# Performance work log

Hardware: AMD Instinct MI355X
Metric: run time of the kernel (lower is better)

The kernel has to match this reference:

```python
import jax, jax.numpy as jnp
import numpy as np

B, S, E, H = 1, 4096, 768, 12
D = E // H  # head_dim = 64


def setup_inputs() -> dict:
    key = jax.random.key(0)
    ks = jax.random.split(key, 9)
    s = 1.0 / np.sqrt(E)
    return {
        "x": jax.random.normal(ks[0], (B, S, E), dtype=jnp.float32),
        "Wq": jax.random.uniform(ks[1], (E, E), jnp.float32, -s, s),
        "bq": jax.random.uniform(ks[2], (E,), jnp.float32, -s, s),
        "Wk": jax.random.uniform(ks[3], (E, E), jnp.float32, -s, s),
        "bk": jax.random.uniform(ks[4], (E,), jnp.float32, -s, s),
        "Wv": jax.random.uniform(ks[5], (E, E), jnp.float32, -s, s),
        "bv": jax.random.uniform(ks[6], (E,), jnp.float32, -s, s),
        "Wo": jax.random.uniform(ks[7], (E, E), jnp.float32, -s, s),
        "bo": jax.random.uniform(ks[8], (E,), jnp.float32, -s, s),
    }


def reference(x, Wq, bq, Wk, bk, Wv, bv, Wo, bo):
    b, s, e = x.shape
    # QKV projections, split heads -> [b, h, s, d]
    def split(t):
        return t.reshape(b, s, H, D).transpose(0, 2, 1, 3)
    q = split(x @ Wq.T + bq)
    k = split(x @ Wk.T + bk)
    v = split(x @ Wv.T + bv)
    scores = jnp.einsum("bhqd,bhkd->bhqk", q, k) / jnp.sqrt(jnp.float32(D))
    attn = jax.nn.softmax(scores, axis=-1)  # dropout is identity in eval
    out = jnp.einsum("bhqk,bhkd->bhqd", attn, v)
    out = out.transpose(0, 2, 1, 3).reshape(b, s, e)
    return out @ Wo.T + bo
```

## Files before the change

kernel.cpp:

```cpp
#include <hip/hip_runtime.h>
#include <hip/hip_bf16.h>
#include <math.h>

#define SEQ 4096
#define EDIM 768
#define NHEAD 12
#define HDIM 64
#define SE (SEQ * EDIM)
#define WMAT (EDIM * EDIM)
#define QSCALE 0.180336880111f

typedef __attribute__((ext_vector_type(8))) __bf16 bf16x8;
typedef __attribute__((ext_vector_type(4))) float f32x4;
typedef __attribute__((ext_vector_type(8))) unsigned short u16x8;
typedef unsigned short ushort_t;
typedef unsigned int uint_t;

#define MFMA16(a, b, c) __builtin_amdgcn_mfma_f32_16x16x32_bf16(a, b, c, 0, 0, 0)
#define GLOAD_LDS16(g, l)                                          \
  __builtin_amdgcn_global_load_lds(                                \
      (const __attribute__((address_space(1))) void*)(g),          \
      (__attribute__((address_space(3))) void*)(l), 16, 0, 0)

__device__ __forceinline__ unsigned short bfbits(float x) {
  return __builtin_bit_cast(unsigned short, (__bf16)x);
}
__device__ __forceinline__ void split1(float x, unsigned short* h,
                                       unsigned short* l) {
  __bf16 hb = (__bf16)x;
  *h = __builtin_bit_cast(unsigned short, hb);
  *l = __builtin_bit_cast(unsigned short, (__bf16)(x - (float)hb));
}
__device__ __forceinline__ bf16x8 ones8() {
  u16x8 u;
#pragma unroll
  for (int e = 0; e < 8; ++e) u[e] = 0x3F80;
  return __builtin_bit_cast(bf16x8, u);
}
__device__ __forceinline__ float exp2_hw(float x) {
  float r;
  asm("v_exp_f32 %0, %1" : "=v"(r) : "v"(x));
  return r;
}

__global__ __launch_bounds__(256) void wprep_kernel(
    const float* __restrict__ W0, const float* __restrict__ W1,
    const float* __restrict__ W2, const float* __restrict__ W3,
    ushort_t* __restrict__ WB, ushort_t* __restrict__ WOH,
    ushort_t* __restrict__ WOL) {
  const int m = blockIdx.y;
  const float* src = (m == 0) ? W0 : (m == 1) ? W1 : (m == 2) ? W2 : W3;
  const size_t i = ((size_t)blockIdx.x * 256 + threadIdx.x) * 8;
  float4 a = *(const float4*)(src + i);
  float4 b = *(const float4*)(src + i + 4);
  float fv[8] = {a.x, a.y, a.z, a.w, b.x, b.y, b.z, b.w};
  if (m < 3) {
    u16x8 hh;
#pragma unroll
    for (int e = 0; e < 8; ++e) hh[e] = bfbits(fv[e]);
    *(u16x8*)(WB + (size_t)m * WMAT + i) = hh;
  } else {
    u16x8 hh, ll;
#pragma unroll
    for (int e = 0; e < 8; ++e) {
      unsigned short x, y;
      split1(fv[e], &x, &y);
      hh[e] = x;
      ll[e] = y;
    }
    *(u16x8*)(WOH + i) = hh;
    *(u16x8*)(WOL + i) = ll;
  }
}

__global__ __launch_bounds__(256) void xprep_kernel(
    const float* __restrict__ x, ushort_t* __restrict__ xb) {
  const size_t i = ((size_t)blockIdx.x * 256 + threadIdx.x) * 8;
  float4 a = *(const float4*)(x + i);
  float4 b = *(const float4*)(x + i + 4);
  float fv[8] = {a.x, a.y, a.z, a.w, b.x, b.y, b.z, b.w};
  u16x8 hh;
#pragma unroll
  for (int e = 0; e < 8; ++e) hh[e] = bfbits(fv[e]);
  *(u16x8*)(xb + i) = hh;
}

__global__ __launch_bounds__(256) void vtrans_kernel(
    const ushort_t* __restrict__ VB, ushort_t* __restrict__ VT) {
  __shared__ ushort_t T[64][65];
  const int t = threadIdx.x;
  const int s0 = blockIdx.x * 64;
  const int hoff = blockIdx.y * 64;
  const int r = t >> 2, c = (t & 3) * 16;
  u16x8 a = *(const u16x8*)(VB + (size_t)(s0 + r) * EDIM + hoff + c);
  u16x8 b = *(const u16x8*)(VB + (size_t)(s0 + r) * EDIM + hoff + c + 8);
#pragma unroll
  for (int e = 0; e < 8; ++e) {
    T[r][c + e] = a[e];
    T[r][c + 8 + e] = b[e];
  }
  __syncthreads();
  u16x8 w0, w1;
#pragma unroll
  for (int e = 0; e < 8; ++e) {
    w0[e] = T[c + e][r];
    w1[e] = T[c + 8 + e][r];
  }
  *(u16x8*)(VT + (size_t)(hoff + r) * SEQ + s0 + c) = w0;
  *(u16x8*)(VT + (size_t)(hoff + r) * SEQ + s0 + c + 8) = w1;
}

__global__ __launch_bounds__(256) void qkv_kernel(
    const ushort_t* __restrict__ XB, const ushort_t* __restrict__ WB,
    const float* __restrict__ bq, const float* __restrict__ bk,
    const float* __restrict__ bv, ushort_t* __restrict__ QB,
    ushort_t* __restrict__ KB, ushort_t* __restrict__ VB) {
  __shared__ __align__(16) ushort_t AS[128][32];
  __shared__ __align__(16) ushort_t BS[128][32];

  const int z = blockIdx.z;
  const ushort_t* Bmat = WB + (size_t)z * WMAT;
  const float* bias = (z == 0) ? bq : (z == 1) ? bk : bv;
  ushort_t* outp = (z == 0) ? QB : (z == 1) ? KB : VB;
  const float scale = (z == 0) ? QSCALE : 1.0f;

  const int t = threadIdx.x;
  const int lane = t & 63;
  const int w = t >> 6;
  const int tn = t & 15;
  const int g = (t >> 4) & 3;
  const int wr = w >> 1, wc = w & 1;
  const int m0 = blockIdx.x * 128;
  const int n0 = blockIdx.y * 128;

  f32x4 acc[4][4];
#pragma unroll
  for (int mi = 0; mi < 4; ++mi)
#pragma unroll
    for (int nj = 0; nj < 4; ++nj) acc[mi][nj] = (f32x4){0.f, 0.f, 0.f, 0.f};

  const int crow = lane >> 2;
  const int ccol = (lane & 3) * 8;

  for (int k0 = 0; k0 < EDIM; k0 += 32) {
    __syncthreads();
#pragma unroll
    for (int i = 0; i < 2; ++i) {
      const int ch = w + 4 * i;
      const int row = ch * 16 + crow;
      GLOAD_LDS16(XB + (size_t)(m0 + row) * EDIM + k0 + ccol, &AS[ch * 16][0]);
      GLOAD_LDS16(Bmat + (size_t)(n0 + row) * EDIM + k0 + ccol, &BS[ch * 16][0]);
    }
    __syncthreads();

    bf16x8 ah[4], bh[4];
#pragma unroll
    for (int mi = 0; mi < 4; ++mi)
      ah[mi] = __builtin_bit_cast(
          bf16x8, *(const u16x8*)&AS[wr * 64 + mi * 16 + tn][8 * g]);
#pragma unroll
    for (int nj = 0; nj < 4; ++nj)
      bh[nj] = __builtin_bit_cast(
          bf16x8, *(const u16x8*)&BS[wc * 64 + nj * 16 + tn][8 * g]);
#pragma unroll
    for (int mi = 0; mi < 4; ++mi)
#pragma unroll
      for (int nj = 0; nj < 4; ++nj)
        acc[mi][nj] = MFMA16(ah[mi], bh[nj], acc[mi][nj]);
  }

#pragma unroll
  for (int mi = 0; mi < 4; ++mi) {
    const int rb = m0 + wr * 64 + mi * 16 + 4 * g;
#pragma unroll
    for (int nj = 0; nj < 4; ++nj) {
      const int col = n0 + wc * 64 + nj * 16 + tn;
      const float bb = bias[col];
#pragma unroll
      for (int r = 0; r < 4; ++r)
        outp[(size_t)(rb + r) * EDIM + col] =
            bfbits((acc[mi][nj][r] + bb) * scale);
    }
  }
}

__global__ __launch_bounds__(256) void proj_kernel(
    const ushort_t* __restrict__ Ah, const ushort_t* __restrict__ Al,
    const ushort_t* __restrict__ Bh, const ushort_t* __restrict__ Bl,
    const float* __restrict__ bias, float* __restrict__ outf) {
  __shared__ __align__(16) ushort_t AhS[128][32];
  __shared__ __align__(16) ushort_t AlS[128][32];
  __shared__ __align__(16) ushort_t BhS[128][32];
  __shared__ __align__(16) ushort_t BlS[128][32];

  const int t = threadIdx.x;
  const int lane = t & 63;
  const int w = t >> 6;
  const int tn = t & 15;
  const int g = (t >> 4) & 3;
  const int wr = w >> 1, wc = w & 1;
  const int m0 = blockIdx.x * 128;
  const int n0 = blockIdx.y * 128;

  f32x4 acc[4][4];
#pragma unroll
  for (int mi = 0; mi < 4; ++mi)
#pragma unroll
    for (int nj = 0; nj < 4; ++nj) acc[mi][nj] = (f32x4){0.f, 0.f, 0.f, 0.f};

  const int crow = lane >> 2;
  const int ccol = (lane & 3) * 8;

  for (int k0 = 0; k0 < EDIM; k0 += 32) {
    __syncthreads();
#pragma unroll
    for (int i = 0; i < 2; ++i) {
      const int ch = w + 4 * i;
      const int row = ch * 16 + crow;
      const size_t ga = (size_t)(m0 + row) * EDIM + k0 + ccol;
      const size_t gb = (size_t)(n0 + row) * EDIM + k0 + ccol;
      GLOAD_LDS16(Ah + ga, &AhS[ch * 16][0]);
      GLOAD_LDS16(Al + ga, &AlS[ch * 16][0]);
      GLOAD_LDS16(Bh + gb, &BhS[ch * 16][0]);
      GLOAD_LDS16(Bl + gb, &BlS[ch * 16][0]);
    }
    __syncthreads();

    bf16x8 ah[4], al[4], bh[4], bl[4];
#pragma unroll
    for (int mi = 0; mi < 4; ++mi) {
      ah[mi] = __builtin_bit_cast(
          bf16x8, *(const u16x8*)&AhS[wr * 64 + mi * 16 + tn][8 * g]);
      al[mi] = __builtin_bit_cast(
          bf16x8, *(const u16x8*)&AlS[wr * 64 + mi * 16 + tn][8 * g]);
    }
#pragma unroll
    for (int nj = 0; nj < 4; ++nj) {
      bh[nj] = __builtin_bit_cast(
          bf16x8, *(const u16x8*)&BhS[wc * 64 + nj * 16 + tn][8 * g]);
      bl[nj] = __builtin_bit_cast(
          bf16x8, *(const u16x8*)&BlS[wc * 64 + nj * 16 + tn][8 * g]);
    }
#pragma unroll
    for (int mi = 0; mi < 4; ++mi)
#pragma unroll
      for (int nj = 0; nj < 4; ++nj)
        acc[mi][nj] = MFMA16(ah[mi], bh[nj], acc[mi][nj]);
#pragma unroll
    for (int mi = 0; mi < 4; ++mi)
#pragma unroll
      for (int nj = 0; nj < 4; ++nj)
        acc[mi][nj] = MFMA16(al[mi], bh[nj], acc[mi][nj]);
#pragma unroll
    for (int mi = 0; mi < 4; ++mi)
#pragma unroll
      for (int nj = 0; nj < 4; ++nj)
        acc[mi][nj] = MFMA16(ah[mi], bl[nj], acc[mi][nj]);
  }

#pragma unroll
  for (int mi = 0; mi < 4; ++mi) {
    const int rb = m0 + wr * 64 + mi * 16 + 4 * g;
#pragma unroll
    for (int nj = 0; nj < 4; ++nj) {
      const int col = n0 + wc * 64 + nj * 16 + tn;
      const float bb = bias[col];
#pragma unroll
      for (int r = 0; r < 4; ++r)
        outf[(size_t)(rb + r) * EDIM + col] = acc[mi][nj][r] + bb;
    }
  }
}

__global__ __launch_bounds__(256) void attn_kernel(
    const ushort_t* __restrict__ QB, const ushort_t* __restrict__ KBg,
    const ushort_t* __restrict__ VTg, ushort_t* __restrict__ Ch_g,
    ushort_t* __restrict__ Cl_g) {
  __shared__ __align__(16) ushort_t KS[2][64][64];
  __shared__ __align__(16) ushort_t VS[2][64][64];
  __shared__ __align__(16) ushort_t Ps[4][16][72];

  const int t = threadIdx.x;
  const int lane = t & 63;
  const int tn = t & 15;
  const int g = (t >> 4) & 3;
  const int kg = g * 8;
  const int wid = t >> 6;
  const int h = blockIdx.y;
  const int q0 = blockIdx.x * 64;
  const int hoff = h * HDIM;

  bf16x8 qb[2];
  {
    const size_t qoff = (size_t)(q0 + 16 * wid + tn) * EDIM + hoff;
    qb[0] = __builtin_bit_cast(bf16x8, *(const u16x8*)(QB + qoff + kg));
    qb[1] = __builtin_bit_cast(bf16x8, *(const u16x8*)(QB + qoff + 32 + kg));
  }

  const int srow = lane >> 3;
  const int sxor = ((lane & 7) ^ srow) << 4;
  const int rswz = (tn & 7) << 4;
  const int off0 = (16 * g) ^ rswz;
  const int off1 = (64 + 16 * g) ^ rswz;

  const bf16x8 ones = ones8();
  f32x4 o[4], lsum;
#pragma unroll
  for (int j = 0; j < 4; ++j) o[j] = (f32x4){0.f, 0.f, 0.f, 0.f};
  lsum = (f32x4){0.f, 0.f, 0.f, 0.f};

#pragma unroll
  for (int c = 0; c < 2; ++c) {
    const int row = 16 * wid + 8 * c + srow;
    GLOAD_LDS16((const char*)(KBg + (size_t)row * EDIM + hoff) + sxor,
                &KS[0][16 * wid + 8 * c][0]);
    GLOAD_LDS16((const char*)(VTg + (size_t)(hoff + row) * SEQ) + sxor,
                &VS[0][16 * wid + 8 * c][0]);
  }

  for (int it = 0; it < SEQ / 64; ++it) {
    const int buf = it & 1;
    __syncthreads();

    if (it + 1 < SEQ / 64) {
      const int k0n = (it + 1) * 64;
#pragma unroll
      for (int c = 0; c < 2; ++c) {
        const int row = 16 * wid + 8 * c + srow;
        GLOAD_LDS16(
            (const char*)(KBg + (size_t)(k0n + row) * EDIM + hoff) + sxor,
            &KS[buf ^ 1][16 * wid + 8 * c][0]);
        GLOAD_LDS16(
            (const char*)(VTg + (size_t)(hoff + row) * SEQ + k0n) + sxor,
            &VS[buf ^ 1][16 * wid + 8 * c][0]);
      }
    }

    f32x4 s[4];
#pragma unroll
    for (int kb = 0; kb < 4; ++kb) {
      const char* krow = (const char*)&KS[buf][16 * kb + tn][0];
      const bf16x8 ka =
          __builtin_bit_cast(bf16x8, *(const u16x8*)(krow + off0));
      const bf16x8 kc =
          __builtin_bit_cast(bf16x8, *(const u16x8*)(krow + off1));
      s[kb] = (f32x4){0.f, 0.f, 0.f, 0.f};
      s[kb] = MFMA16(ka, qb[0], s[kb]);
      s[kb] = MFMA16(kc, qb[1], s[kb]);
    }

#pragma unroll
    for (int kb = 0; kb < 4; ++kb) {
      uint2 pk;
      pk.x = (uint_t)bfbits(exp2_hw(s[kb][0])) |
             ((uint_t)bfbits(exp2_hw(s[kb][1])) << 16);
      pk.y = (uint_t)bfbits(exp2_hw(s[kb][2])) |
             ((uint_t)bfbits(exp2_hw(s[kb][3])) << 16);
      *(uint2*)&Ps[wid][tn][16 * kb + 4 * g] = pk;
    }

    const bf16x8 pa0 =
        __builtin_bit_cast(bf16x8, *(const u16x8*)&Ps[wid][tn][kg]);
    const bf16x8 pa1 =
        __builtin_bit_cast(bf16x8, *(const u16x8*)&Ps[wid][tn][32 + kg]);

#pragma unroll
    for (int j = 0; j < 4; ++j) {
      const char* vrow = (const char*)&VS[buf][16 * j + tn][0];
      const bf16x8 v0 =
          __builtin_bit_cast(bf16x8, *(const u16x8*)(vrow + off0));
      const bf16x8 v1 =
          __builtin_bit_cast(bf16x8, *(const u16x8*)(vrow + off1));
      o[j] = MFMA16(pa0, v0, o[j]);
      o[j] = MFMA16(pa1, v1, o[j]);
    }
    lsum = MFMA16(pa0, ones, lsum);
    lsum = MFMA16(pa1, ones, lsum);
  }

#pragma unroll
  for (int r = 0; r < 4; ++r) {
    const float inv = 1.f / lsum[r];
#pragma unroll
    for (int j = 0; j < 4; ++j) {
      const float val = o[j][r] * inv;
      unsigned short hh, ll;
      split1(val, &hh, &ll);
      const size_t idx =
          (size_t)(q0 + 16 * wid + 4 * g + r) * EDIM + hoff + 16 * j + tn;
      Ch_g[idx] = hh;
      Cl_g[idx] = ll;
    }
  }
}

extern "C" void kernel_launch(void* const* d_in, const int* in_sizes, int n_in,
                              void* d_out, int out_size, void* d_ws,
                              size_t ws_size, hipStream_t stream) {
  const float* x  = (const float*)d_in[0];
  const float* Wq = (const float*)d_in[1];
  const float* bq = (const float*)d_in[2];
  const float* Wk = (const float*)d_in[3];
  const float* bk = (const float*)d_in[4];
  const float* Wv = (const float*)d_in[5];
  const float* bv = (const float*)d_in[6];
  const float* Wo = (const float*)d_in[7];
  const float* bo = (const float*)d_in[8];
  float* out = (float*)d_out;

  ushort_t* WB  = (ushort_t*)d_ws;
  ushort_t* WOH = WB + (size_t)3 * WMAT;
  ushort_t* WOL = WOH + (size_t)WMAT;
  ushort_t* XB  = WOL + (size_t)WMAT;
  ushort_t* QB  = XB + (size_t)SE;
  ushort_t* KB  = QB + (size_t)SE;
  ushort_t* VB  = KB + (size_t)SE;
  ushort_t* VT  = VB + (size_t)SE;
  ushort_t* CH  = VT + (size_t)SE;
  ushort_t* CL  = CH + (size_t)SE;

  dim3 gw(WMAT / 2048, 4);
  wprep_kernel<<<gw, 256, 0, stream>>>(Wq, Wk, Wv, Wo, WB, WOH, WOL);
  xprep_kernel<<<SE / 2048, 256, 0, stream>>>(x, XB);

  dim3 gq(SEQ / 128, EDIM / 128, 3);
  qkv_kernel<<<gq, 256, 0, stream>>>(XB, WB, bq, bk, bv, QB, KB, VB);

  dim3 gt(SEQ / 64, NHEAD);
  vtrans_kernel<<<gt, 256, 0, stream>>>(VB, VT);

  dim3 ga(SEQ / 64, NHEAD);
  attn_kernel<<<ga, 256, 0, stream>>>(QB, KB, VT, CH, CL);

  dim3 go(SEQ / 128, EDIM / 128);
  proj_kernel<<<go, 256, 0, stream>>>(CH, CL, WOH, WOL, bo, out);
}
```

Measured before the change: 167.4 us.

## Use 32x32 MFMA in attention with split-K waves; fuse V transpose into QKV epilogue

The attention kernel moves from 16x16x32 to 32x32x16 MFMA tiles. Each wave now handles 32 queries against half of each key block, and the two partial results are reduced through LDS at the end. The P fragment is built in registers with cvt_pk_bf16 and permlane32_swap, removing the per-iteration LDS round trip for P. The separate V transpose kernel is dropped: the QKV kernel writes V directly in transposed layout, which saves one launch and one pass over V in memory at the cost of strided 8-byte stores.

```diff
diff --git a/kernel.cpp b/kernel.cpp
--- a/kernel.cpp
+++ b/kernel.cpp
@@ -12,11 +12,14 @@
 
 typedef __attribute__((ext_vector_type(8))) __bf16 bf16x8;
 typedef __attribute__((ext_vector_type(4))) float f32x4;
+typedef __attribute__((ext_vector_type(16))) float f32x16;
 typedef __attribute__((ext_vector_type(8))) unsigned short u16x8;
+typedef __attribute__((ext_vector_type(4))) unsigned short u16x4;
 typedef unsigned short ushort_t;
 typedef unsigned int uint_t;
 
 #define MFMA16(a, b, c) __builtin_amdgcn_mfma_f32_16x16x32_bf16(a, b, c, 0, 0, 0)
+#define MFMA32(a, b, c) __builtin_amdgcn_mfma_f32_32x32x16_bf16(a, b, c, 0, 0, 0)
 #define GLOAD_LDS16(g, l)                                          \
   __builtin_amdgcn_global_load_lds(                                \
       (const __attribute__((address_space(1))) void*)(g),          \
@@ -40,6 +43,11 @@
 __device__ __forceinline__ float exp2_hw(float x) {
   float r;
   asm("v_exp_f32 %0, %1" : "=v"(r) : "v"(x));
+  return r;
+}
+__device__ __forceinline__ uint_t cvtpk(float a, float b) {
+  uint_t r;
+  asm("v_cvt_pk_bf16_f32 %0, %1, %2" : "=v"(r) : "v"(a), "v"(b));
   return r;
 }
 
@@ -85,43 +93,18 @@
   *(u16x8*)(xb + i) = hh;
 }
 
-__global__ __launch_bounds__(256) void vtrans_kernel(
-    const ushort_t* __restrict__ VB, ushort_t* __restrict__ VT) {
-  __shared__ ushort_t T[64][65];
-  const int t = threadIdx.x;
-  const int s0 = blockIdx.x * 64;
-  const int hoff = blockIdx.y * 64;
-  const int r = t >> 2, c = (t & 3) * 16;
-  u16x8 a = *(const u16x8*)(VB + (size_t)(s0 + r) * EDIM + hoff + c);
-  u16x8 b = *(const u16x8*)(VB + (size_t)(s0 + r) * EDIM + hoff + c + 8);
-#pragma unroll
-  for (int e = 0; e < 8; ++e) {
-    T[r][c + e] = a[e];
-    T[r][c + 8 + e] = b[e];
-  }
-  __syncthreads();
-  u16x8 w0, w1;
-#pragma unroll
-  for (int e = 0; e < 8; ++e) {
-    w0[e] = T[c + e][r];
-    w1[e] = T[c + 8 + e][r];
-  }
-  *(u16x8*)(VT + (size_t)(hoff + r) * SEQ + s0 + c) = w0;
-  *(u16x8*)(VT + (size_t)(hoff + r) * SEQ + s0 + c + 8) = w1;
-}
-
 __global__ __launch_bounds__(256) void qkv_kernel(
     const ushort_t* __restrict__ XB, const ushort_t* __restrict__ WB,
     const float* __restrict__ bq, const float* __restrict__ bk,
     const float* __restrict__ bv, ushort_t* __restrict__ QB,
-    ushort_t* __restrict__ KB, ushort_t* __restrict__ VB) {
+    ushort_t* __restrict__ KB, ushort_t* __restrict__ VT) {
   __shared__ __align__(16) ushort_t AS[128][32];
   __shared__ __align__(16) ushort_t BS[128][32];
 
   const int z = blockIdx.z;
   const ushort_t* Bmat = WB + (size_t)z * WMAT;
   const float* bias = (z == 0) ? bq : (z == 1) ? bk : bv;
-  ushort_t* outp = (z == 0) ? QB : (z == 1) ? KB : VB;
+  ushort_t* outp = (z == 0) ? QB : (z == 1) ? KB : VT;
   const float scale = (z == 0) ? QSCALE : 1.0f;
 
   const int t = threadIdx.x;
@@ -176,10 +159,17 @@
     for (int nj = 0; nj < 4; ++nj) {
       const int col = n0 + wc * 64 + nj * 16 + tn;
       const float bb = bias[col];
-#pragma unroll
-      for (int r = 0; r < 4; ++r)
-        outp[(size_t)(rb + r) * EDIM + col] =
-            bfbits((acc[mi][nj][r] + bb) * scale);
+      if (z == 2) {
+        u16x4 pk;
+#pragma unroll
+        for (int r = 0; r < 4; ++r) pk[r] = bfbits(acc[mi][nj][r] + bb);
+        *(u16x4*)(outp + (size_t)col * SEQ + rb) = pk;
+      } else {
+#pragma unroll
+        for (int r = 0; r < 4; ++r)
+          outp[(size_t)(rb + r) * EDIM + col] =
+              bfbits((acc[mi][nj][r] + bb) * scale);
+      }
     }
   }
 }
@@ -278,36 +268,37 @@
     ushort_t* __restrict__ Cl_g) {
   __shared__ __align__(16) ushort_t KS[2][64][64];
   __shared__ __align__(16) ushort_t VS[2][64][64];
-  __shared__ __align__(16) ushort_t Ps[4][16][72];
 
   const int t = threadIdx.x;
   const int lane = t & 63;
-  const int tn = t & 15;
-  const int g = (t >> 4) & 3;
-  const int kg = g * 8;
+  const int l31 = lane & 31;
+  const int hi = lane >> 5;
   const int wid = t >> 6;
-  const int h = blockIdx.y;
+  const int wq = wid & 1;
+  const int wk = wid >> 1;
   const int q0 = blockIdx.x * 64;
-  const int hoff = h * HDIM;
-
-  bf16x8 qb[2];
+  const int hoff = blockIdx.y * HDIM;
+
+  bf16x8 qf[4];
   {
-    const size_t qoff = (size_t)(q0 + 16 * wid + tn) * EDIM + hoff;
-    qb[0] = __builtin_bit_cast(bf16x8, *(const u16x8*)(QB + qoff + kg));
-    qb[1] = __builtin_bit_cast(bf16x8, *(const u16x8*)(QB + qoff + 32 + kg));
+    const ushort_t* qp =
+        QB + (size_t)(q0 + 32 * wq + l31) * EDIM + hoff + 8 * hi;
+#pragma unroll
+    for (int s4 = 0; s4 < 4; ++s4)
+      qf[s4] = __builtin_bit_cast(bf16x8, *(const u16x8*)(qp + 16 * s4));
   }
 
   const int srow = lane >> 3;
   const int sxor = ((lane & 7) ^ srow) << 4;
-  const int rswz = (tn & 7) << 4;
-  const int off0 = (16 * g) ^ rswz;
-  const int off1 = (64 + 16 * g) ^ rswz;
 
   const bf16x8 ones = ones8();
-  f32x4 o[4], lsum;
-#pragma unroll
-  for (int j = 0; j < 4; ++j) o[j] = (f32x4){0.f, 0.f, 0.f, 0.f};
-  lsum = (f32x4){0.f, 0.f, 0.f, 0.f};
+  f32x16 O0, O1, LS;
+#pragma unroll
+  for (int r = 0; r < 16; ++r) {
+    O0[r] = 0.f;
+    O1[r] = 0.f;
+    LS[r] = 0.f;
+  }
 
 #pragma unroll
   for (int c = 0; c < 2; ++c) {
@@ -317,6 +308,9 @@
     GLOAD_LDS16((const char*)(VTg + (size_t)(hoff + row) * SEQ) + sxor,
                 &VS[0][16 * wid + 8 * c][0]);
   }
+
+  const int krow = 32 * wk + l31;
+  const int kswz = (krow & 7) << 4;
 
   for (int it = 0; it < SEQ / 64; ++it) {
     const int buf = it & 1;
@@ -336,60 +330,105 @@
       }
     }
 
-    f32x4 s[4];
-#pragma unroll
-    for (int kb = 0; kb < 4; ++kb) {
-      const char* krow = (const char*)&KS[buf][16 * kb + tn][0];
-      const bf16x8 ka =
-          __builtin_bit_cast(bf16x8, *(const u16x8*)(krow + off0));
-      const bf16x8 kc =
-          __builtin_bit_cast(bf16x8, *(const u16x8*)(krow + off1));
-      s[kb] = (f32x4){0.f, 0.f, 0.f, 0.f};
-      s[kb] = MFMA16(ka, qb[0], s[kb]);
-      s[kb] = MFMA16(kc, qb[1], s[kb]);
-    }
-
-#pragma unroll
-    for (int kb = 0; kb < 4; ++kb) {
-      uint2 pk;
-      pk.x = (uint_t)bfbits(exp2_hw(s[kb][0])) |
-             ((uint_t)bfbits(exp2_hw(s[kb][1])) << 16);
-      pk.y = (uint_t)bfbits(exp2_hw(s[kb][2])) |
-             ((uint_t)bfbits(exp2_hw(s[kb][3])) << 16);
-      *(uint2*)&Ps[wid][tn][16 * kb + 4 * g] = pk;
-    }
-
-    const bf16x8 pa0 =
-        __builtin_bit_cast(bf16x8, *(const u16x8*)&Ps[wid][tn][kg]);
-    const bf16x8 pa1 =
-        __builtin_bit_cast(bf16x8, *(const u16x8*)&Ps[wid][tn][32 + kg]);
-
+    f32x16 s;
+#pragma unroll
+    for (int r = 0; r < 16; ++r) s[r] = 0.f;
+    {
+      const char* kb = (const char*)&KS[buf][krow][0];
+#pragma unroll
+      for (int st = 0; st < 4; ++st) {
+        const bf16x8 kf = __builtin_bit_cast(
+            bf16x8, *(const u16x8*)(kb + ((32 * st + 16 * hi) ^ kswz)));
+        s = MFMA32(kf, qf[st], s);
+      }
+    }
+
+#pragma unroll
+    for (int r = 0; r < 16; ++r) s[r] = exp2_hw(s[r]);
+
+    uint_t w0 = cvtpk(s[0], s[1]), w1 = cvtpk(s[2], s[3]);
+    uint_t w2 = cvtpk(s[4], s[5]), w3 = cvtpk(s[6], s[7]);
+    uint_t w4 = cvtpk(s[8], s[9]), w5 = cvtpk(s[10], s[11]);
+    uint_t w6 = cvtpk(s[12], s[13]), w7 = cvtpk(s[14], s[15]);
+    asm("v_permlane32_swap_b32 %0, %1" : "+v"(w0), "+v"(w2));
+    asm("v_permlane32_swap_b32 %0, %1" : "+v"(w1), "+v"(w3));
+    asm("v_permlane32_swap_b32 %0, %1" : "+v"(w4), "+v"(w6));
+    asm("v_permlane32_swap_b32 %0, %1" : "+v"(w5), "+v"(w7));
+    const bf16x8 pa0 = __builtin_bit_cast(bf16x8, (uint4){w0, w1, w2, w3});
+    const bf16x8 pa1 = __builtin_bit_cast(bf16x8, (uint4){w4, w5, w6, w7});
+
+#pragma unroll
+    for (int db = 0; db < 2; ++db) {
+      const int vrow = 32 * db + l31;
+      const int vswz = (vrow & 7) << 4;
+      const char* vb = (const char*)&VS[buf][vrow][0];
+      const bf16x8 vf0 = __builtin_bit_cast(
+          bf16x8, *(const u16x8*)(vb + ((64 * wk + 16 * hi) ^ vswz)));
+      const bf16x8 vf1 = __builtin_bit_cast(
+          bf16x8, *(const u16x8*)(vb + ((64 * wk + 32 + 16 * hi) ^ vswz)));
+      if (db == 0) {
+        O0 = MFMA32(pa0, vf0, O0);
+        O0 = MFMA32(pa1, vf1, O0);
+      } else {
+        O1 = MFMA32(pa0, vf0, O1);
+        O1 = MFMA32(pa1, vf1, O1);
+      }
+    }
+    LS = MFMA32(pa0, ones, LS);
+    LS = MFMA32(pa1, ones, LS);
+  }
+
+  float(*OLt)[64][32] = (float(*)[64][32]) & KS[0][0][0];
+  float(*LT)[32] = (float(*)[32]) & VS[0][0][0];
+
+  __syncthreads();
+  if (wk == 1) {
 #pragma unroll
     for (int j = 0; j < 4; ++j) {
-      const char* vrow = (const char*)&VS[buf][16 * j + tn][0];
-      const bf16x8 v0 =
-          __builtin_bit_cast(bf16x8, *(const u16x8*)(vrow + off0));
-      const bf16x8 v1 =
-          __builtin_bit_cast(bf16x8, *(const u16x8*)(vrow + off1));
-      o[j] = MFMA16(pa0, v0, o[j]);
-      o[j] = MFMA16(pa1, v1, o[j]);
-    }
-    lsum = MFMA16(pa0, ones, lsum);
-    lsum = MFMA16(pa1, ones, lsum);
-  }
-
-#pragma unroll
-  for (int r = 0; r < 4; ++r) {
-    const float inv = 1.f / lsum[r];
+      *(float4*)&OLt[wq][l31][8 * j + 4 * hi] =
+          make_float4(O0[4 * j], O0[4 * j + 1], O0[4 * j + 2], O0[4 * j + 3]);
+      *(float4*)&OLt[wq][32 + l31][8 * j + 4 * hi] =
+          make_float4(O1[4 * j], O1[4 * j + 1], O1[4 * j + 2], O1[4 * j + 3]);
+    }
+    if (l31 == 0) {
+#pragma unroll
+      for (int j = 0; j < 4; ++j)
+        *(float4*)&LT[wq][8 * j + 4 * hi] = make_float4(
+            LS[4 * j], LS[4 * j + 1], LS[4 * j + 2], LS[4 * j + 3]);
+    }
+  }
+  __syncthreads();
+  if (wk == 0) {
+    float linv[16];
 #pragma unroll
     for (int j = 0; j < 4; ++j) {
-      const float val = o[j][r] * inv;
-      unsigned short hh, ll;
-      split1(val, &hh, &ll);
-      const size_t idx =
-          (size_t)(q0 + 16 * wid + 4 * g + r) * EDIM + hoff + 16 * j + tn;
-      Ch_g[idx] = hh;
-      Cl_g[idx] = ll;
+      const float4 lv = *(const float4*)&LT[wq][8 * j + 4 * hi];
+      linv[4 * j + 0] = 1.f / (LS[4 * j + 0] + lv.x);
+      linv[4 * j + 1] = 1.f / (LS[4 * j + 1] + lv.y);
+      linv[4 * j + 2] = 1.f / (LS[4 * j + 2] + lv.z);
+      linv[4 * j + 3] = 1.f / (LS[4 * j + 3] + lv.w);
+    }
+#pragma unroll
+    for (int db = 0; db < 2; ++db) {
+      const f32x16 Od = db ? O1 : O0;
+#pragma unroll
+      for (int j = 0; j < 4; ++j) {
+        const float4 ov = *(const float4*)&OLt[wq][32 * db + l31][8 * j + 4 * hi];
+        const float vals[4] = {(Od[4 * j + 0] + ov.x) * linv[4 * j + 0],
+                               (Od[4 * j + 1] + ov.y) * linv[4 * j + 1],
+                               (Od[4 * j + 2] + ov.z) * linv[4 * j + 2],
+                               (Od[4 * j + 3] + ov.w) * linv[4 * j + 3]};
+#pragma unroll
+        for (int e = 0; e < 4; ++e) {
+          unsigned short hh, ll;
+          split1(vals[e], &hh, &ll);
+          const size_t idx =
+              (size_t)(q0 + 32 * wq + 8 * j + 4 * hi + e) * EDIM + hoff +
+              32 * db + l31;
+          Ch_g[idx] = hh;
+          Cl_g[idx] = ll;
+        }
+      }
     }
   }
 }
@@ -414,8 +453,7 @@
   ushort_t* XB  = WOL + (size_t)WMAT;
   ushort_t* QB  = XB + (size_t)SE;
   ushort_t* KB  = QB + (size_t)SE;
-  ushort_t* VB  = KB + (size_t)SE;
-  ushort_t* VT  = VB + (size_t)SE;
+  ushort_t* VT  = KB + (size_t)SE;
   ushort_t* CH  = VT + (size_t)SE;
   ushort_t* CL  = CH + (size_t)SE;
 
@@ -424,10 +462,7 @@
   xprep_kernel<<<SE / 2048, 256, 0, stream>>>(x, XB);
 
   dim3 gq(SEQ / 128, EDIM / 128, 3);
-  qkv_kernel<<<gq, 256, 0, stream>>>(XB, WB, bq, bk, bv, QB, KB, VB);
-
-  dim3 gt(SEQ / 64, NHEAD);
-  vtrans_kernel<<<gt, 256, 0, stream>>>(VB, VT);
+  qkv_kernel<<<gq, 256, 0, stream>>>(XB, WB, bq, bk, bv, QB, KB, VT);
 
   dim3 ga(SEQ / 64, NHEAD);
   attn_kernel<<<ga, 256, 0, stream>>>(QB, KB, VT, CH, CL);
```

Measured after the change: 186.7 us. +11.5%, slower.
